# Performance work log

Hardware: AMD Instinct MI355X
Metric: run time of the kernel (lower is better)

## Reference

```python
import jax, jax.numpy as jnp
import numpy as np

B, LQ, LF, NW, NFR, E, D, V = 4, 128, 64, 2, 8, 128, 128, 64


def _project(x, W, b):
    # torch Emb_Projection('linear'): Linear then zero-row mask
    y = x @ W + b
    m = 1.0 - jnp.all(y == 0, axis=-1, keepdims=True).astype(y.dtype)
    return y * m


def setup_inputs() -> dict:
    key = jax.random.key(0)
    ks = jax.random.split(key, 12)
    s = lambda k, shape, fan: jax.random.normal(k, shape, jnp.float32) / np.sqrt(fan)
    return {
        "query": jax.random.normal(ks[0], (B, LQ, E), jnp.float32),
        "fragment": jax.random.normal(ks[1], (B, NW, NFR, LF, E), jnp.float32),
        "query_mask": jnp.ones((B, LQ), jnp.float32),
        "fragment_mask": jnp.ones((B, NW, NFR, LF), jnp.float32),
        # learned params (stored [in, out]; torch Linear is x @ W.T with W [out,in])
        "proj_W": s(ks[2], (E, D), E),
        "proj_b": jnp.zeros((D,), jnp.float32),
        "self_att_W": s(ks[3], (NW, D), D),   # n_way Linear(D,1,bias=False)
        "q_att_W": s(ks[4], (D, V), D),
        "f_att_W": s(ks[5], (D, V), D),
        "qf_att_W": s(ks[6], (D, V), D),
        "gate_w": s(ks[7], (V,), V),          # value_gate: Linear(V,1,bias=False)
        "val_w": s(ks[8], (V,), V),           # value_att:  Linear(V,1,bias=False)
    }


def reference(query, fragment, query_mask, fragment_mask, proj_W, proj_b,
              self_att_W, q_att_W, f_att_W, qf_att_W, gate_w, val_w):
    query = _project(query, proj_W, proj_b)          # [B,Lq,D]
    fragment = _project(fragment, proj_W, proj_b)    # [B,NW,NFR,Lf,D]

    # (1) fragment self-attention -> frag_code
    logits = jnp.einsum('bwfld,wd->bwfl', fragment, self_att_W)   # per-way Linear(D,1)
    e = jnp.exp(logits) * fragment_mask
    frag_self_att = e / (e.sum(-1, keepdims=True) + 1e-7)          # [B,NW,NFR,Lf]
    frag_code = (fragment * frag_self_att[..., None]).sum(-2)     # [B,NW,NFR,D]

    # (2) query-to-fragment attention
    frag_r = fragment.reshape(fragment.shape[0], -1, fragment.shape[-2], fragment.shape[-1])  # [B,NF,Lf,D]
    qr = query[:, None]                                            # [B,1,Lq,D]
    q_att = qr @ q_att_W                                           # [B,1,Lq,V]
    f_att = frag_r @ f_att_W                                       # [B,NF,Lf,V]
    # large broadcast product [B,NF,Lf,Lq,D] then project to V
    qf = (qr[:, :, None, :, :] * frag_r[:, :, :, None, :]) @ qf_att_W  # [B,NF,Lf,Lq,V]
    qf = q_att[:, :, None] + f_att[:, :, :, None] + qf
    qf = qf.max(axis=-3)                                           # max over Lf -> [B,NF,Lq,V]

    qf_gate = jax.nn.sigmoid(qf @ gate_w) * query_mask[:, None]    # [B,NF,Lq]
    e2 = jnp.exp(qf @ val_w) * query_mask[:, None]
    qf_norm = e2 / (e2.sum(-1, keepdims=True) + 1e-7)              # [B,NF,Lq]

    query_code = (qr * qf_norm[..., None]).sum(axis=2)             # [B,NF,D]
    query_code = query_code.reshape(frag_code.shape)               # [B,NW,NFR,D]
    return frag_code, query_code, frag_self_att, qf_gate, query
```

## Files before the change

kernel.cpp:

```cpp
#include <hip/hip_runtime.h>
#include <hip/hip_bf16.h>

#define B_   4
#define LQ_  128
#define LF_  64
#define NW_  2
#define NFR_ 8
#define E_   128
#define D_   128
#define V_   64
#define NWF_ (NW_*NFR_)
#define NROW_Q (B_*LQ_)
#define NROW_F (B_*NW_*NFR_*LF_)

using bf16 = __hip_bfloat16;
typedef unsigned short u16;
typedef unsigned int   u32;
typedef __attribute__((ext_vector_type(8))) short  bf16x8;
typedef __attribute__((ext_vector_type(4))) float  f32x4;
typedef __attribute__((ext_vector_type(4))) u32    u32x4;

#define WS_QP    0
#define WS_QATT  65536
#define WS_E2    98304
#define WS_FP16  106496
#define WS_W3T   368640
#define WS_WFT   372736
#define WS_PWT   376832
#define WS_QAT   385024

#define OUT_FRAGCODE  0
#define OUT_QUERYCODE 8192
#define OUT_SELFATT   16384
#define OUT_QFGATE    20480
#define OUT_QUERY     28672

__device__ __forceinline__ float us2f(u16 v) { return __uint_as_float((u32)v << 16); }
__device__ __forceinline__ float lo2f(u32 v) { return __uint_as_float(v << 16); }
__device__ __forceinline__ float hi2f(u32 v) { return __uint_as_float(v & 0xffff0000u); }
__device__ __forceinline__ u16 f2b_raw(float f) {
    u32 u = __float_as_uint(f);
    return (u16)((u + 0x7fffu + ((u >> 16) & 1u)) >> 16);
}
__device__ __forceinline__ u32 pk2(float hi, float lo) {
    return __builtin_amdgcn_perm(__float_as_uint(hi), __float_as_uint(lo), 0x07060302u);
}
template<bool BF> __device__ __forceinline__ float LD(const void* p, int i) {
    return BF ? us2f(((const u16*)p)[i]) : ((const float*)p)[i];
}
template<bool BF> __device__ __forceinline__ void ST(void* p, int i, float v) {
    if (BF) ((u16*)p)[i] = f2b_raw(v); else ((float*)p)[i] = v;
}
template<bool BF> __device__ __forceinline__ u16 LDB(const void* p, int i) {
    return BF ? ((const u16*)p)[i] : f2b_raw(((const float*)p)[i]);
}
__device__ __forceinline__ bool is_bf(const void* qmask) {
    return ((const u16*)qmask)[0] == 0x3F80u;
}

template<bool BF>
__device__ __forceinline__ void prep_body(const void* src, u16* dst, u16* stg, int N)
{
    int t = threadIdx.x;
    int st = N + 1, total = 128 * N;
    for (int i = t; i < total; i += 256)
        stg[(i / N) * st + (i % N)] = LDB<BF>(src, i);
    __syncthreads();
    for (int j = t; j < total; j += 256) {
        int n = j >> 7, k = j & 127;
        dst[n * 128 + k] = stg[k * st + n];
    }
}
__global__ __launch_bounds__(256) void k_prep(
    const void* projW, const void* qattW, const void* qfW, const void* fattW,
    const void* qmask, float* ws)
{
    __shared__ u16 stg[128 * 129];
    int bx = blockIdx.x;
    const void* src = (bx == 0) ? projW : (bx == 1) ? qattW : (bx == 2) ? qfW : fattW;
    u16* dst = (u16*)(ws + ((bx == 0) ? WS_PWT : (bx == 1) ? WS_QAT : (bx == 2) ? WS_W3T : WS_WFT));
    int N = (bx == 0) ? 128 : 64;
    if (is_bf(qmask)) prep_body<true >(src, dst, stg, N);
    else              prep_body<false>(src, dst, stg, N);
}

template<bool BF>
__device__ __forceinline__ void proj_body(
    const void* query, const void* fragment, const void* projB,
    float* ws, void* out, u16* s_y)
{
    int r = blockIdx.x, t = threadIdx.x;
    int lane = t & 63, wave = t >> 6, m = lane & 15, quad = lane >> 4;
    bool isq = (r >= 256);
    int base = isq ? (r - 256) * 16 : r * 16;
    const void* x = isq ? query : fragment;
    const u16* pwt = (const u16*)(ws + WS_PWT);

    bf16x8 af[4];
    #pragma unroll
    for (int kt = 0; kt < 4; ++kt) {
        int off = (base + m) * 128 + kt * 32 + quad * 8;
        if (BF) af[kt] = *(const bf16x8*)((const u16*)x + off);
        else {
            f32x4 a = *(const f32x4*)((const float*)x + off);
            f32x4 c = *(const f32x4*)((const float*)x + off + 4);
            u32x4 av;
            av.x = pk2(a.y, a.x); av.y = pk2(a.w, a.z);
            av.z = pk2(c.y, c.x); av.w = pk2(c.w, c.z);
            af[kt] = __builtin_bit_cast(bf16x8, av);
        }
    }
    int nt0 = wave * 2;
    f32x4 acc[2];
    #pragma unroll
    for (int i = 0; i < 2; ++i) {
        float bv = LD<BF>(projB, (nt0 + i) * 16 + m);
        acc[i] = (f32x4){bv, bv, bv, bv};
    }
    #pragma unroll
    for (int kt = 0; kt < 4; ++kt)
        #pragma unroll
        for (int i = 0; i < 2; ++i) {
            bf16x8 bfr = *(const bf16x8*)(pwt + ((nt0 + i) * 16 + m) * 128 + kt * 32 + quad * 8);
            acc[i] = __builtin_amdgcn_mfma_f32_16x16x32_bf16(af[kt], bfr, acc[i], 0, 0, 0);
        }
    if (!isq) {
        u16* fp16 = (u16*)(ws + WS_FP16);
        #pragma unroll
        for (int i = 0; i < 2; ++i)
            #pragma unroll
            for (int rr = 0; rr < 4; ++rr)
                fp16[(size_t)(base + quad * 4 + rr) * 128 + (nt0 + i) * 16 + m] = f2b_raw(acc[i][rr]);
    } else {
        #pragma unroll
        for (int i = 0; i < 2; ++i)
            #pragma unroll
            for (int rr = 0; rr < 4; ++rr) {
                int gr = base + quad * 4 + rr, col = (nt0 + i) * 16 + m;
                float v = acc[i][rr];
                ws[WS_QP + (size_t)gr * 128 + col] = v;
                ST<BF>(out, OUT_QUERY + gr * 128 + col, v);
                s_y[(quad * 4 + rr) * 132 + col] = f2b_raw(v);
            }
        __syncthreads();
        bf16x8 ay[4];
        #pragma unroll
        for (int kt = 0; kt < 4; ++kt)
            ay[kt] = *(const bf16x8*)&s_y[m * 132 + kt * 32 + quad * 8];
        const u16* qat = (const u16*)(ws + WS_QAT);
        f32x4 a2 = (f32x4){0.f, 0.f, 0.f, 0.f};
        #pragma unroll
        for (int kt = 0; kt < 4; ++kt) {
            bf16x8 b2 = *(const bf16x8*)(qat + (wave * 16 + m) * 128 + kt * 32 + quad * 8);
            a2 = __builtin_amdgcn_mfma_f32_16x16x32_bf16(ay[kt], b2, a2, 0, 0, 0);
        }
        #pragma unroll
        for (int rr = 0; rr < 4; ++rr)
            ws[WS_QATT + (size_t)(base + quad * 4 + rr) * 64 + wave * 16 + m] = a2[rr];
    }
}
__global__ __launch_bounds__(256) void k_proj(
    const void* query, const void* fragment, const void* projB, const void* qmask,
    float* ws, void* out)
{
    __shared__ u16 s_y[16 * 132];
    if (is_bf(qmask)) proj_body<true >(query, fragment, projB, ws, out, s_y);
    else              proj_body<false>(query, fragment, projB, ws, out, s_y);
}

template<bool BF>
__device__ __forceinline__ void qf_body(
    const void* saW, const void* fmask, const void* gatew, const void* valw,
    const void* qmask, float* ws, void* out, char* smem)
{
    u16*   s_fp  = (u16*)smem;
    u16*   s_fa  = (u16*)(smem + 16384);
    float* s_saw = (float*)(smem + 34816);
    float* s_att = (float*)(smem + 35328);
    float* s_tmp = (float*)(smem + 35584);

    int t = threadIdx.x, lane = t & 63, wave = t >> 6;
    int bwf = blockIdx.x >> 2, qt2 = blockIdx.x & 3;
    int b = bwf >> 4;
    int m = lane & 15, quad = lane >> 4;
    int lq = wave >> 1, qsub = wave & 1;
    int sk = (m & 7) << 3;

    {
        const u32* src = (const u32*)((const u16*)(ws + WS_FP16)) + (size_t)bwf * 4096;
        u32* d32 = (u32*)s_fp;
        #pragma unroll
        for (int k = 0; k < 16; ++k) {
            int i = t + 512 * k;
            int row = i >> 6, cp = i & 63;
            d32[row * 64 + (cp ^ ((row & 7) << 2))] = src[i];
        }
    }
    const u16* w3t = (const u16*)(ws + WS_W3T);
    bf16x8 w3f[4][4];
    #pragma unroll
    for (int vt = 0; vt < 4; ++vt)
        #pragma unroll
        for (int kt = 0; kt < 4; ++kt)
            w3f[vt][kt] = *(const bf16x8*)(w3t + (vt * 16 + m) * 128 + kt * 32 + quad * 8);
    __syncthreads();

    int lbase = lq * 16;
    if (qsub == 0) {
        const u16* wft = (const u16*)(ws + WS_WFT);
        bf16x8 afk[4];
        #pragma unroll
        for (int kt = 0; kt < 4; ++kt)
            afk[kt] = *(const bf16x8*)&s_fp[(lbase + m) * 128 + ((kt * 32 + quad * 8) ^ sk)];
        #pragma unroll
        for (int vt = 0; vt < 4; ++vt) {
            bf16x8 wf = *(const bf16x8*)(wft + (vt * 16 + m) * 128 + 0 * 32 + quad * 8);
            f32x4 a0 = (f32x4){0.f, 0.f, 0.f, 0.f};
            #pragma unroll
            for (int kt = 0; kt < 4; ++kt) {
                bf16x8 wk = *(const bf16x8*)(wft + (vt * 16 + m) * 128 + kt * 32 + quad * 8);
                a0 = __builtin_amdgcn_mfma_f32_16x16x32_bf16(afk[kt], wk, a0, 0, 0, 0);
                (void)wf;
            }
            #pragma unroll
            for (int r = 0; r < 4; ++r)
                s_fa[(lbase + quad * 4 + r) * 72 + vt * 16 + m] = f2b_raw(a0[r]);
        }
    }
    float qpreg[4][8];
    {
        const float* qprow = ws + WS_QP + (size_t)(b * LQ_ + qt2 * 32 + qsub * 16 + m) * 128;
        #pragma unroll
        for (int kt = 0; kt < 4; ++kt) {
            f32x4 x0 = *(const f32x4*)(qprow + kt * 32 + quad * 8);
            f32x4 x1 = *(const f32x4*)(qprow + kt * 32 + quad * 8 + 4);
            qpreg[kt][0] = x0.x; qpreg[kt][1] = x0.y; qpreg[kt][2] = x0.z; qpreg[kt][3] = x0.w;
            qpreg[kt][4] = x1.x; qpreg[kt][5] = x1.y; qpreg[kt][6] = x1.z; qpreg[kt][7] = x1.w;
        }
    }
    __syncthreads();

    float mx[4][4];
    #pragma unroll
    for (int vt = 0; vt < 4; ++vt)
        #pragma unroll
        for (int r = 0; r < 4; ++r) mx[vt][r] = -1e30f;

    u32x4 fvc[4], fvn[4];
    #pragma unroll
    for (int kt = 0; kt < 4; ++kt)
        fvc[kt] = *(const u32x4*)&s_fp[lbase * 128 + (kt * 32 + quad * 8)];
    #pragma unroll 2
    for (int li = 0; li < 16; ++li) {
        if (li < 15) {
            int l2 = lbase + li + 1;
            #pragma unroll
            for (int kt = 0; kt < 4; ++kt)
                fvn[kt] = *(const u32x4*)&s_fp[l2 * 128 + ((kt * 32 + quad * 8) ^ (((li + 1) & 7) << 3))];
        }
        int l = lbase + li;
        bf16x8 af[4];
        #pragma unroll
        for (int kt = 0; kt < 4; ++kt) {
            u32x4 fv = fvc[kt];
            u32x4 av;
            av.x = pk2(qpreg[kt][1] * hi2f(fv.x), qpreg[kt][0] * lo2f(fv.x));
            av.y = pk2(qpreg[kt][3] * hi2f(fv.y), qpreg[kt][2] * lo2f(fv.y));
            av.z = pk2(qpreg[kt][5] * hi2f(fv.z), qpreg[kt][4] * lo2f(fv.z));
            av.w = pk2(qpreg[kt][7] * hi2f(fv.w), qpreg[kt][6] * lo2f(fv.w));
            af[kt] = __builtin_bit_cast(bf16x8, av);
        }
        #pragma unroll
        for (int vt = 0; vt < 4; ++vt) {
            float fa = us2f(s_fa[l * 72 + vt * 16 + m]);
            f32x4 acc = (f32x4){fa, fa, fa, fa};
            #pragma unroll
            for (int kt = 0; kt < 4; ++kt)
                acc = __builtin_amdgcn_mfma_f32_16x16x32_bf16(af[kt], w3f[vt][kt], acc, 0, 0, 0);
            #pragma unroll
            for (int r = 0; r < 4; ++r) mx[vt][r] = fmaxf(mx[vt][r], acc[r]);
        }
        #pragma unroll
        for (int kt = 0; kt < 4; ++kt) fvc[kt] = fvn[kt];
    }
    __syncthreads();
    #pragma unroll
    for (int vt = 0; vt < 4; ++vt)
        #pragma unroll
        for (int r = 0; r < 4; ++r)
            s_fa[(lq * 32 + qsub * 16 + quad * 4 + r) * 72 + vt * 16 + m] = f2b_raw(mx[vt][r]);
    __syncthreads();

    {
        int q = t >> 4, vg = t & 15;
        int gq = qt2 * 32 + q;
        float gp = 0.f, ep = 0.f;
        #pragma unroll
        for (int jj = 0; jj < 4; ++jj) {
            int v = vg * 4 + jj;
            float mval = -1e30f;
            #pragma unroll
            for (int w = 0; w < 4; ++w)
                mval = fmaxf(mval, us2f(s_fa[(w * 32 + q) * 72 + v]));
            float qf = mval + ws[WS_QATT + (size_t)(b * LQ_ + gq) * 64 + v];
            gp += qf * LD<BF>(gatew, v);
            ep += qf * LD<BF>(valw, v);
        }
        #pragma unroll
        for (int off = 1; off <= 8; off <<= 1) {
            gp += __shfl_xor(gp, off, 64);
            ep += __shfl_xor(ep, off, 64);
        }
        if (vg == 0) {
            float qm = LD<BF>(qmask, b * LQ_ + gq);
            float g = (1.0f / (1.0f + expf(-gp))) * qm;
            ST<BF>(out, OUT_QFGATE + bwf * LQ_ + gq, g);
            ws[WS_E2 + bwf * LQ_ + gq] = expf(ep) * qm;
        }
    }

    if (qt2 == 0) {
        if (t < 128) s_saw[t] = LD<BF>(saW, ((bwf >> 3) & 1) * 128 + t);
        __syncthreads();
        int l = t >> 3, j8 = t & 7;
        int swz = (l & 7) << 3;
        float p = 0.f;
        #pragma unroll
        for (int seg = 0; seg < 2; ++seg) {
            int koff = j8 * 16 + seg * 8;
            u32x4 fv = *(const u32x4*)&s_fp[l * 128 + (koff ^ swz)];
            const float* swp = &s_saw[koff];
            p += lo2f(fv.x) * swp[0] + hi2f(fv.x) * swp[1]
               + lo2f(fv.y) * swp[2] + hi2f(fv.y) * swp[3]
               + lo2f(fv.z) * swp[4] + hi2f(fv.z) * swp[5]
               + lo2f(fv.w) * swp[6] + hi2f(fv.w) * swp[7];
        }
        p += __shfl_xor(p, 1, 64);
        p += __shfl_xor(p, 2, 64);
        p += __shfl_xor(p, 4, 64);
        if (j8 == 0) s_att[l] = expf(p) * LD<BF>(fmask, bwf * LF_ + l);
        __syncthreads();
        if (t < 64) {
            float e = s_att[t], s = e;
            #pragma unroll
            for (int off = 1; off <= 32; off <<= 1) s += __shfl_xor(s, off, 64);
            float nrm = e / (s + 1e-7f);
            s_att[t] = nrm;
            ST<BF>(out, OUT_SELFATT + bwf * LF_ + t, nrm);
        }
        __syncthreads();
        int d = t & 127, grp = t >> 7;
        float fc = 0.f;
        #pragma unroll
        for (int li2 = 0; li2 < 16; ++li2) {
            int l2 = grp * 16 + li2;
            fc += us2f(s_fp[l2 * 128 + (d ^ ((l2 & 7) << 3))]) * s_att[l2];
        }
        s_tmp[grp * 128 + d] = fc;
        __syncthreads();
        if (t < 128)
            ST<BF>(out, OUT_FRAGCODE + bwf * D_ + t,
                   s_tmp[t] + s_tmp[128 + t] + s_tmp[256 + t] + s_tmp[384 + t]);
    }
}
__global__ __launch_bounds__(512) void k_qf(
    const void* saW, const void* fmask, const void* gatew, const void* valw,
    const void* qmask, float* ws, void* out)
{
    __shared__ char smem[37632];
    if (is_bf(qmask)) qf_body<true >(saW, fmask, gatew, valw, qmask, ws, out, smem);
    else              qf_body<false>(saW, fmask, gatew, valw, qmask, ws, out, smem);
}

template<bool BF>
__device__ __forceinline__ void qcode_body(const float* ws, void* out,
                                           float* s_n, float* s_part)
{
    int bwf = blockIdx.x, b = bwf >> 4, t = threadIdx.x;
    float e = ws[WS_E2 + bwf * LQ_ + t];
    float s = e;
    #pragma unroll
    for (int off = 1; off <= 32; off <<= 1) s += __shfl_xor(s, off, 64);
    if ((t & 63) == 0) s_part[t >> 6] = s;
    __syncthreads();
    float tot = s_part[0] + s_part[1] + 1e-7f;
    s_n[t] = e / tot;
    __syncthreads();
    float qc = 0.f;
    #pragma unroll 8
    for (int q = 0; q < LQ_; ++q)
        qc += ws[WS_QP + (size_t)(b * LQ_ + q) * 128 + t] * s_n[q];
    ST<BF>(out, OUT_QUERYCODE + bwf * D_ + t, qc);
}
__global__ __launch_bounds__(128) void k_qcode(const void* qmask, const float* ws, void* out)
{
    __shared__ float s_n[LQ_];
    __shared__ float s_part[2];
    if (is_bf(qmask)) qcode_body<true >(ws, out, s_n, s_part);
    else              qcode_body<false>(ws, out, s_n, s_part);
}

extern "C" void kernel_launch(void* const* d_in, const int* in_sizes, int n_in,
                              void* d_out, int out_size, void* d_ws, size_t ws_size,
                              hipStream_t stream)
{
    const void* query    = d_in[0];
    const void* fragment = d_in[1];
    const void* qmask    = d_in[2];
    const void* fmask    = d_in[3];
    const void* projW    = d_in[4];
    const void* projB    = d_in[5];
    const void* saW      = d_in[6];
    const void* qattW    = d_in[7];
    const void* fattW    = d_in[8];
    const void* qfW      = d_in[9];
    const void* gatew    = d_in[10];
    const void* valw     = d_in[11];
    float* ws = (float*)d_ws;

    hipLaunchKernelGGL(k_prep, dim3(4), dim3(256), 0, stream,
                       projW, qattW, qfW, fattW, qmask, ws);
    hipLaunchKernelGGL(k_proj, dim3(288), dim3(256), 0, stream,
                       query, fragment, projB, qmask, ws, d_out);
    hipLaunchKernelGGL(k_qf, dim3(256), dim3(512), 0, stream,
                       saW, fmask, gatew, valw, qmask, ws, d_out);
    hipLaunchKernelGGL(k_qcode, dim3(B_ * NWF_), dim3(128), 0, stream,
                       qmask, ws, d_out);
}
```

Measured before the change: 114.2 us.

## Fuse all four kernels into one per-fragment block kernel

Replaces the prep, projection, qf and qcode kernels with a single kernel that launches one 512-thread block per (batch, fragment). Each block recomputes the query projection for its batch, projects its own fragment, and keeps everything in shared memory, so there are no workspace round trips and no extra launches. It also reads weights directly with strided gathers instead of using pre-transposed copies. The trade-offs are redundant query-projection work across the 16 blocks of each batch, a drop from 256 blocks to 64 (less parallelism), and each wave now looping over all 64 fragment rows rather than 16.

```diff
diff --git a/kernel.cpp b/kernel.cpp
--- a/kernel.cpp
+++ b/kernel.cpp
@@ -10,8 +10,6 @@
 #define D_   128
 #define V_   64
 #define NWF_ (NW_*NFR_)
-#define NROW_Q (B_*LQ_)
-#define NROW_F (B_*NW_*NFR_*LF_)
 
 using bf16 = __hip_bfloat16;
 typedef unsigned short u16;
@@ -20,20 +18,22 @@
 typedef __attribute__((ext_vector_type(4))) float  f32x4;
 typedef __attribute__((ext_vector_type(4))) u32    u32x4;
 
-#define WS_QP    0
-#define WS_QATT  65536
-#define WS_E2    98304
-#define WS_FP16  106496
-#define WS_W3T   368640
-#define WS_WFT   372736
-#define WS_PWT   376832
-#define WS_QAT   385024
-
 #define OUT_FRAGCODE  0
 #define OUT_QUERYCODE 8192
 #define OUT_SELFATT   16384
 #define OUT_QFGATE    20480
 #define OUT_QUERY     28672
+
+#define L_FP   0
+#define L_QP   16384
+#define L_FA   49152
+#define L_E2   58368
+#define L_N    58880
+#define L_SAW  59392
+#define L_ATT  59904
+#define L_RED  60160
+#define L_PART 62208
+#define L_TOT  62240
 
 __device__ __forceinline__ float us2f(u16 v) { return __uint_as_float((u32)v << 16); }
 __device__ __forceinline__ float lo2f(u32 v) { return __uint_as_float(v << 16); }
@@ -57,212 +57,152 @@
 __device__ __forceinline__ bool is_bf(const void* qmask) {
     return ((const u16*)qmask)[0] == 0x3F80u;
 }
-
 template<bool BF>
-__device__ __forceinline__ void prep_body(const void* src, u16* dst, u16* stg, int N)
+__device__ __forceinline__ bf16x8 loadA(const void* x, int row, int kt, int quad) {
+    int off = row * 128 + kt * 32 + quad * 8;
+    if (BF) return *(const bf16x8*)((const u16*)x + off);
+    f32x4 a = *(const f32x4*)((const float*)x + off);
+    f32x4 c = *(const f32x4*)((const float*)x + off + 4);
+    u32x4 av;
+    av.x = pk2(a.y, a.x); av.y = pk2(a.w, a.z);
+    av.z = pk2(c.y, c.x); av.w = pk2(c.w, c.z);
+    return __builtin_bit_cast(bf16x8, av);
+}
+template<bool BF>
+__device__ __forceinline__ bf16x8 ldBf(const void* W, int N, int n, int k0) {
+    short tmp[8];
+    #pragma unroll
+    for (int j = 0; j < 8; ++j) tmp[j] = (short)LDB<BF>(W, (k0 + j) * N + n);
+    bf16x8 f;
+    #pragma unroll
+    for (int j = 0; j < 8; ++j) f[j] = tmp[j];
+    return f;
+}
+
+template<bool BF>
+__device__ __forceinline__ void main_body(
+    const void* query, const void* fragment, const void* qmask, const void* fmask,
+    const void* projW, const void* projB, const void* saW, const void* qattW,
+    const void* fattW, const void* qfW, const void* gatew, const void* valw,
+    void* out, char* smem)
 {
-    int t = threadIdx.x;
-    int st = N + 1, total = 128 * N;
-    for (int i = t; i < total; i += 256)
-        stg[(i / N) * st + (i % N)] = LDB<BF>(src, i);
-    __syncthreads();
-    for (int j = t; j < total; j += 256) {
-        int n = j >> 7, k = j & 127;
-        dst[n * 128 + k] = stg[k * st + n];
-    }
-}
-__global__ __launch_bounds__(256) void k_prep(
-    const void* projW, const void* qattW, const void* qfW, const void* fattW,
-    const void* qmask, float* ws)
-{
-    __shared__ u16 stg[128 * 129];
-    int bx = blockIdx.x;
-    const void* src = (bx == 0) ? projW : (bx == 1) ? qattW : (bx == 2) ? qfW : fattW;
-    u16* dst = (u16*)(ws + ((bx == 0) ? WS_PWT : (bx == 1) ? WS_QAT : (bx == 2) ? WS_W3T : WS_WFT));
-    int N = (bx == 0) ? 128 : 64;
-    if (is_bf(qmask)) prep_body<true >(src, dst, stg, N);
-    else              prep_body<false>(src, dst, stg, N);
-}
-
-template<bool BF>
-__device__ __forceinline__ void proj_body(
-    const void* query, const void* fragment, const void* projB,
-    float* ws, void* out, u16* s_y)
-{
-    int r = blockIdx.x, t = threadIdx.x;
-    int lane = t & 63, wave = t >> 6, m = lane & 15, quad = lane >> 4;
-    bool isq = (r >= 256);
-    int base = isq ? (r - 256) * 16 : r * 16;
-    const void* x = isq ? query : fragment;
-    const u16* pwt = (const u16*)(ws + WS_PWT);
-
-    bf16x8 af[4];
+    u16*   s_fp   = (u16*)(smem + L_FP);
+    u16*   s_qp   = (u16*)(smem + L_QP);
+    u16*   s_fa   = (u16*)(smem + L_FA);
+    float* s_e2   = (float*)(smem + L_E2);
+    float* s_n    = (float*)(smem + L_N);
+    float* s_saw  = (float*)(smem + L_SAW);
+    float* s_att  = (float*)(smem + L_ATT);
+    float* s_red  = (float*)(smem + L_RED);
+    float* s_part = (float*)(smem + L_PART);
+
+    int bwf = blockIdx.x, b = bwf >> 4;
+    int t = threadIdx.x, lane = t & 63, w = t >> 6;
+    int m = lane & 15, quad = lane >> 4;
+    int sk = (m & 7) << 3;
+
+    {
+        bool dofp = (w < 4);
+        bf16x8 af_q[4], af_f[4];
+        #pragma unroll
+        for (int kt = 0; kt < 4; ++kt)
+            af_q[kt] = loadA<BF>(query, b * 128 + w * 16 + m, kt, quad);
+        if (dofp)
+            #pragma unroll
+            for (int kt = 0; kt < 4; ++kt)
+                af_f[kt] = loadA<BF>(fragment, bwf * 64 + w * 16 + m, kt, quad);
+        #pragma unroll
+        for (int nt = 0; nt < 8; ++nt) {
+            int n = nt * 16 + m;
+            bf16x8 bw[4];
+            #pragma unroll
+            for (int kt = 0; kt < 4; ++kt) bw[kt] = ldBf<BF>(projW, 128, n, kt * 32 + quad * 8);
+            float bv = LD<BF>(projB, n);
+            f32x4 aq = (f32x4){bv, bv, bv, bv};
+            #pragma unroll
+            for (int kt = 0; kt < 4; ++kt)
+                aq = __builtin_amdgcn_mfma_f32_16x16x32_bf16(af_q[kt], bw[kt], aq, 0, 0, 0);
+            #pragma unroll
+            for (int rr = 0; rr < 4; ++rr) {
+                int row = w * 16 + quad * 4 + rr;
+                s_qp[row * 128 + (n ^ ((row & 7) << 3))] = f2b_raw(aq[rr]);
+            }
+            if (dofp) {
+                f32x4 afc = (f32x4){bv, bv, bv, bv};
+                #pragma unroll
+                for (int kt = 0; kt < 4; ++kt)
+                    afc = __builtin_amdgcn_mfma_f32_16x16x32_bf16(af_f[kt], bw[kt], afc, 0, 0, 0);
+                #pragma unroll
+                for (int rr = 0; rr < 4; ++rr) {
+                    int row = w * 16 + quad * 4 + rr;
+                    s_fp[row * 128 + (n ^ ((row & 7) << 3))] = f2b_raw(afc[rr]);
+                }
+            }
+        }
+    }
+    __syncthreads();
+
+    bf16x8 aq2[4];
+    #pragma unroll
+    for (int kt = 0; kt < 4; ++kt)
+        aq2[kt] = *(const bf16x8*)&s_qp[(w * 16 + m) * 128 + ((kt * 32 + quad * 8) ^ sk)];
+    f32x4 qat[4];
+    #pragma unroll
+    for (int vt = 0; vt < 4; ++vt) {
+        qat[vt] = (f32x4){0.f, 0.f, 0.f, 0.f};
+        #pragma unroll
+        for (int kt = 0; kt < 4; ++kt) {
+            bf16x8 bb = ldBf<BF>(qattW, 64, vt * 16 + m, kt * 32 + quad * 8);
+            qat[vt] = __builtin_amdgcn_mfma_f32_16x16x32_bf16(aq2[kt], bb, qat[vt], 0, 0, 0);
+        }
+    }
+    float qpreg[4][8];
     #pragma unroll
     for (int kt = 0; kt < 4; ++kt) {
-        int off = (base + m) * 128 + kt * 32 + quad * 8;
-        if (BF) af[kt] = *(const bf16x8*)((const u16*)x + off);
-        else {
-            f32x4 a = *(const f32x4*)((const float*)x + off);
-            f32x4 c = *(const f32x4*)((const float*)x + off + 4);
-            u32x4 av;
-            av.x = pk2(a.y, a.x); av.y = pk2(a.w, a.z);
-            av.z = pk2(c.y, c.x); av.w = pk2(c.w, c.z);
-            af[kt] = __builtin_bit_cast(bf16x8, av);
-        }
-    }
-    int nt0 = wave * 2;
-    f32x4 acc[2];
-    #pragma unroll
-    for (int i = 0; i < 2; ++i) {
-        float bv = LD<BF>(projB, (nt0 + i) * 16 + m);
-        acc[i] = (f32x4){bv, bv, bv, bv};
-    }
-    #pragma unroll
-    for (int kt = 0; kt < 4; ++kt)
-        #pragma unroll
-        for (int i = 0; i < 2; ++i) {
-            bf16x8 bfr = *(const bf16x8*)(pwt + ((nt0 + i) * 16 + m) * 128 + kt * 32 + quad * 8);
-            acc[i] = __builtin_amdgcn_mfma_f32_16x16x32_bf16(af[kt], bfr, acc[i], 0, 0, 0);
-        }
-    if (!isq) {
-        u16* fp16 = (u16*)(ws + WS_FP16);
-        #pragma unroll
-        for (int i = 0; i < 2; ++i)
-            #pragma unroll
-            for (int rr = 0; rr < 4; ++rr)
-                fp16[(size_t)(base + quad * 4 + rr) * 128 + (nt0 + i) * 16 + m] = f2b_raw(acc[i][rr]);
-    } else {
-        #pragma unroll
-        for (int i = 0; i < 2; ++i)
-            #pragma unroll
-            for (int rr = 0; rr < 4; ++rr) {
-                int gr = base + quad * 4 + rr, col = (nt0 + i) * 16 + m;
-                float v = acc[i][rr];
-                ws[WS_QP + (size_t)gr * 128 + col] = v;
-                ST<BF>(out, OUT_QUERY + gr * 128 + col, v);
-                s_y[(quad * 4 + rr) * 132 + col] = f2b_raw(v);
-            }
-        __syncthreads();
-        bf16x8 ay[4];
+        u32x4 uv = __builtin_bit_cast(u32x4, aq2[kt]);
+        qpreg[kt][0] = lo2f(uv.x); qpreg[kt][1] = hi2f(uv.x);
+        qpreg[kt][2] = lo2f(uv.y); qpreg[kt][3] = hi2f(uv.y);
+        qpreg[kt][4] = lo2f(uv.z); qpreg[kt][5] = hi2f(uv.z);
+        qpreg[kt][6] = lo2f(uv.w); qpreg[kt][7] = hi2f(uv.w);
+    }
+    if (w < 4) {
+        bf16x8 afa[4];
         #pragma unroll
         for (int kt = 0; kt < 4; ++kt)
-            ay[kt] = *(const bf16x8*)&s_y[m * 132 + kt * 32 + quad * 8];
-        const u16* qat = (const u16*)(ws + WS_QAT);
-        f32x4 a2 = (f32x4){0.f, 0.f, 0.f, 0.f};
+            afa[kt] = *(const bf16x8*)&s_fp[(w * 16 + m) * 128 + ((kt * 32 + quad * 8) ^ sk)];
+        #pragma unroll
+        for (int vt = 0; vt < 4; ++vt) {
+            f32x4 a0 = (f32x4){0.f, 0.f, 0.f, 0.f};
+            #pragma unroll
+            for (int kt = 0; kt < 4; ++kt) {
+                bf16x8 wk = ldBf<BF>(fattW, 64, vt * 16 + m, kt * 32 + quad * 8);
+                a0 = __builtin_amdgcn_mfma_f32_16x16x32_bf16(afa[kt], wk, a0, 0, 0, 0);
+            }
+            #pragma unroll
+            for (int r = 0; r < 4; ++r)
+                s_fa[(w * 16 + quad * 4 + r) * 72 + vt * 16 + m] = f2b_raw(a0[r]);
+        }
+    }
+    bf16x8 w3f[4][4];
+    #pragma unroll
+    for (int vt = 0; vt < 4; ++vt)
+        #pragma unroll
+        for (int kt = 0; kt < 4; ++kt)
+            w3f[vt][kt] = ldBf<BF>(qfW, 64, vt * 16 + m, kt * 32 + quad * 8);
+    __syncthreads();
+
+    float mx[4][4];
+    #pragma unroll
+    for (int vt = 0; vt < 4; ++vt)
+        #pragma unroll
+        for (int r = 0; r < 4; ++r) mx[vt][r] = -1e30f;
+    #pragma unroll 2
+    for (int li = 0; li < 64; ++li) {
+        int sw2 = (li & 7) << 3;
+        bf16x8 af[4];
         #pragma unroll
         for (int kt = 0; kt < 4; ++kt) {
-            bf16x8 b2 = *(const bf16x8*)(qat + (wave * 16 + m) * 128 + kt * 32 + quad * 8);
-            a2 = __builtin_amdgcn_mfma_f32_16x16x32_bf16(ay[kt], b2, a2, 0, 0, 0);
-        }
-        #pragma unroll
-        for (int rr = 0; rr < 4; ++rr)
-            ws[WS_QATT + (size_t)(base + quad * 4 + rr) * 64 + wave * 16 + m] = a2[rr];
-    }
-}
-__global__ __launch_bounds__(256) void k_proj(
-    const void* query, const void* fragment, const void* projB, const void* qmask,
-    float* ws, void* out)
-{
-    __shared__ u16 s_y[16 * 132];
-    if (is_bf(qmask)) proj_body<true >(query, fragment, projB, ws, out, s_y);
-    else              proj_body<false>(query, fragment, projB, ws, out, s_y);
-}
-
-template<bool BF>
-__device__ __forceinline__ void qf_body(
-    const void* saW, const void* fmask, const void* gatew, const void* valw,
-    const void* qmask, float* ws, void* out, char* smem)
-{
-    u16*   s_fp  = (u16*)smem;
-    u16*   s_fa  = (u16*)(smem + 16384);
-    float* s_saw = (float*)(smem + 34816);
-    float* s_att = (float*)(smem + 35328);
-    float* s_tmp = (float*)(smem + 35584);
-
-    int t = threadIdx.x, lane = t & 63, wave = t >> 6;
-    int bwf = blockIdx.x >> 2, qt2 = blockIdx.x & 3;
-    int b = bwf >> 4;
-    int m = lane & 15, quad = lane >> 4;
-    int lq = wave >> 1, qsub = wave & 1;
-    int sk = (m & 7) << 3;
-
-    {
-        const u32* src = (const u32*)((const u16*)(ws + WS_FP16)) + (size_t)bwf * 4096;
-        u32* d32 = (u32*)s_fp;
-        #pragma unroll
-        for (int k = 0; k < 16; ++k) {
-            int i = t + 512 * k;
-            int row = i >> 6, cp = i & 63;
-            d32[row * 64 + (cp ^ ((row & 7) << 2))] = src[i];
-        }
-    }
-    const u16* w3t = (const u16*)(ws + WS_W3T);
-    bf16x8 w3f[4][4];
-    #pragma unroll
-    for (int vt = 0; vt < 4; ++vt)
-        #pragma unroll
-        for (int kt = 0; kt < 4; ++kt)
-            w3f[vt][kt] = *(const bf16x8*)(w3t + (vt * 16 + m) * 128 + kt * 32 + quad * 8);
-    __syncthreads();
-
-    int lbase = lq * 16;
-    if (qsub == 0) {
-        const u16* wft = (const u16*)(ws + WS_WFT);
-        bf16x8 afk[4];
-        #pragma unroll
-        for (int kt = 0; kt < 4; ++kt)
-            afk[kt] = *(const bf16x8*)&s_fp[(lbase + m) * 128 + ((kt * 32 + quad * 8) ^ sk)];
-        #pragma unroll
-        for (int vt = 0; vt < 4; ++vt) {
-            bf16x8 wf = *(const bf16x8*)(wft + (vt * 16 + m) * 128 + 0 * 32 + quad * 8);
-            f32x4 a0 = (f32x4){0.f, 0.f, 0.f, 0.f};
-            #pragma unroll
-            for (int kt = 0; kt < 4; ++kt) {
-                bf16x8 wk = *(const bf16x8*)(wft + (vt * 16 + m) * 128 + kt * 32 + quad * 8);
-                a0 = __builtin_amdgcn_mfma_f32_16x16x32_bf16(afk[kt], wk, a0, 0, 0, 0);
-                (void)wf;
-            }
-            #pragma unroll
-            for (int r = 0; r < 4; ++r)
-                s_fa[(lbase + quad * 4 + r) * 72 + vt * 16 + m] = f2b_raw(a0[r]);
-        }
-    }
-    float qpreg[4][8];
-    {
-        const float* qprow = ws + WS_QP + (size_t)(b * LQ_ + qt2 * 32 + qsub * 16 + m) * 128;
-        #pragma unroll
-        for (int kt = 0; kt < 4; ++kt) {
-            f32x4 x0 = *(const f32x4*)(qprow + kt * 32 + quad * 8);
-            f32x4 x1 = *(const f32x4*)(qprow + kt * 32 + quad * 8 + 4);
-            qpreg[kt][0] = x0.x; qpreg[kt][1] = x0.y; qpreg[kt][2] = x0.z; qpreg[kt][3] = x0.w;
-            qpreg[kt][4] = x1.x; qpreg[kt][5] = x1.y; qpreg[kt][6] = x1.z; qpreg[kt][7] = x1.w;
-        }
-    }
-    __syncthreads();
-
-    float mx[4][4];
-    #pragma unroll
-    for (int vt = 0; vt < 4; ++vt)
-        #pragma unroll
-        for (int r = 0; r < 4; ++r) mx[vt][r] = -1e30f;
-
-    u32x4 fvc[4], fvn[4];
-    #pragma unroll
-    for (int kt = 0; kt < 4; ++kt)
-        fvc[kt] = *(const u32x4*)&s_fp[lbase * 128 + (kt * 32 + quad * 8)];
-    #pragma unroll 2
-    for (int li = 0; li < 16; ++li) {
-        if (li < 15) {
-            int l2 = lbase + li + 1;
-            #pragma unroll
-            for (int kt = 0; kt < 4; ++kt)
-                fvn[kt] = *(const u32x4*)&s_fp[l2 * 128 + ((kt * 32 + quad * 8) ^ (((li + 1) & 7) << 3))];
-        }
-        int l = lbase + li;
-        bf16x8 af[4];
-        #pragma unroll
-        for (int kt = 0; kt < 4; ++kt) {
-            u32x4 fv = fvc[kt];
+            u32x4 fv = *(const u32x4*)&s_fp[li * 128 + ((kt * 32 + quad * 8) ^ sw2)];
             u32x4 av;
             av.x = pk2(qpreg[kt][1] * hi2f(fv.x), qpreg[kt][0] * lo2f(fv.x));
             av.y = pk2(qpreg[kt][3] * hi2f(fv.y), qpreg[kt][2] * lo2f(fv.y));
@@ -272,7 +212,7 @@
         }
         #pragma unroll
         for (int vt = 0; vt < 4; ++vt) {
-            float fa = us2f(s_fa[l * 72 + vt * 16 + m]);
+            float fa = us2f(s_fa[li * 72 + vt * 16 + m]);
             f32x4 acc = (f32x4){fa, fa, fa, fa};
             #pragma unroll
             for (int kt = 0; kt < 4; ++kt)
@@ -280,48 +220,52 @@
             #pragma unroll
             for (int r = 0; r < 4; ++r) mx[vt][r] = fmaxf(mx[vt][r], acc[r]);
         }
-        #pragma unroll
-        for (int kt = 0; kt < 4; ++kt) fvc[kt] = fvn[kt];
-    }
-    __syncthreads();
-    #pragma unroll
-    for (int vt = 0; vt < 4; ++vt)
-        #pragma unroll
-        for (int r = 0; r < 4; ++r)
-            s_fa[(lq * 32 + qsub * 16 + quad * 4 + r) * 72 + vt * 16 + m] = f2b_raw(mx[vt][r]);
-    __syncthreads();
-
-    {
-        int q = t >> 4, vg = t & 15;
-        int gq = qt2 * 32 + q;
-        float gp = 0.f, ep = 0.f;
-        #pragma unroll
-        for (int jj = 0; jj < 4; ++jj) {
-            int v = vg * 4 + jj;
-            float mval = -1e30f;
-            #pragma unroll
-            for (int w = 0; w < 4; ++w)
-                mval = fmaxf(mval, us2f(s_fa[(w * 32 + q) * 72 + v]));
-            float qf = mval + ws[WS_QATT + (size_t)(b * LQ_ + gq) * 64 + v];
-            gp += qf * LD<BF>(gatew, v);
-            ep += qf * LD<BF>(valw, v);
-        }
-        #pragma unroll
-        for (int off = 1; off <= 8; off <<= 1) {
-            gp += __shfl_xor(gp, off, 64);
-            ep += __shfl_xor(ep, off, 64);
-        }
-        if (vg == 0) {
-            float qm = LD<BF>(qmask, b * LQ_ + gq);
-            float g = (1.0f / (1.0f + expf(-gp))) * qm;
-            ST<BF>(out, OUT_QFGATE + bwf * LQ_ + gq, g);
-            ws[WS_E2 + bwf * LQ_ + gq] = expf(ep) * qm;
-        }
-    }
-
-    if (qt2 == 0) {
-        if (t < 128) s_saw[t] = LD<BF>(saW, ((bwf >> 3) & 1) * 128 + t);
-        __syncthreads();
+    }
+
+    {
+        float gwv[4], vwv[4];
+        #pragma unroll
+        for (int vt = 0; vt < 4; ++vt) {
+            gwv[vt] = LD<BF>(gatew, vt * 16 + m);
+            vwv[vt] = LD<BF>(valw, vt * 16 + m);
+        }
+        #pragma unroll
+        for (int r = 0; r < 4; ++r) {
+            float gp = 0.f, ep = 0.f;
+            #pragma unroll
+            for (int vt = 0; vt < 4; ++vt) {
+                float qf = mx[vt][r] + qat[vt][r];
+                gp += qf * gwv[vt];
+                ep += qf * vwv[vt];
+            }
+            #pragma unroll
+            for (int off = 1; off <= 8; off <<= 1) {
+                gp += __shfl_xor(gp, off, 64);
+                ep += __shfl_xor(ep, off, 64);
+            }
+            if (m == 0) {
+                int gq = w * 16 + quad * 4 + r;
+                float qm = LD<BF>(qmask, b * 128 + gq);
+                float g = (1.0f / (1.0f + expf(-gp))) * qm;
+                ST<BF>(out, OUT_QFGATE + bwf * LQ_ + gq, g);
+                s_e2[gq] = expf(ep) * qm;
+            }
+        }
+    }
+
+    if ((bwf & 15) == 0) {
+        #pragma unroll
+        for (int it = 0; it < 32; ++it) {
+            int i = t + 512 * it;
+            int row = i >> 7, col = i & 127;
+            float v = us2f(s_qp[row * 128 + (col ^ ((row & 7) << 3))]);
+            ST<BF>(out, OUT_QUERY + (b * 128 + row) * 128 + col, v);
+        }
+    }
+
+    if (t < 128) s_saw[t] = LD<BF>(saW, ((bwf >> 3) & 1) * 128 + t);
+    __syncthreads();
+    {
         int l = t >> 3, j8 = t & 7;
         int swz = (l & 7) << 3;
         float p = 0.f;
@@ -339,16 +283,18 @@
         p += __shfl_xor(p, 2, 64);
         p += __shfl_xor(p, 4, 64);
         if (j8 == 0) s_att[l] = expf(p) * LD<BF>(fmask, bwf * LF_ + l);
-        __syncthreads();
-        if (t < 64) {
-            float e = s_att[t], s = e;
-            #pragma unroll
-            for (int off = 1; off <= 32; off <<= 1) s += __shfl_xor(s, off, 64);
-            float nrm = e / (s + 1e-7f);
-            s_att[t] = nrm;
-            ST<BF>(out, OUT_SELFATT + bwf * LF_ + t, nrm);
-        }
-        __syncthreads();
+    }
+    __syncthreads();
+    if (t < 64) {
+        float e = s_att[t], s = e;
+        #pragma unroll
+        for (int off = 1; off <= 32; off <<= 1) s += __shfl_xor(s, off, 64);
+        float nrm = e / (s + 1e-7f);
+        s_att[t] = nrm;
+        ST<BF>(out, OUT_SELFATT + bwf * LF_ + t, nrm);
+    }
+    __syncthreads();
+    {
         int d = t & 127, grp = t >> 7;
         float fc = 0.f;
         #pragma unroll
@@ -356,74 +302,65 @@
             int l2 = grp * 16 + li2;
             fc += us2f(s_fp[l2 * 128 + (d ^ ((l2 & 7) << 3))]) * s_att[l2];
         }
-        s_tmp[grp * 128 + d] = fc;
-        __syncthreads();
-        if (t < 128)
-            ST<BF>(out, OUT_FRAGCODE + bwf * D_ + t,
-                   s_tmp[t] + s_tmp[128 + t] + s_tmp[256 + t] + s_tmp[384 + t]);
-    }
-}
-__global__ __launch_bounds__(512) void k_qf(
-    const void* saW, const void* fmask, const void* gatew, const void* valw,
-    const void* qmask, float* ws, void* out)
+        s_red[grp * 128 + d] = fc;
+    }
+    __syncthreads();
+    if (t < 128)
+        ST<BF>(out, OUT_FRAGCODE + bwf * D_ + t,
+               s_red[t] + s_red[128 + t] + s_red[256 + t] + s_red[384 + t]);
+
+    float e2v = 0.f;
+    if (t < 128) {
+        e2v = s_e2[t];
+        float s = e2v;
+        #pragma unroll
+        for (int off = 1; off <= 32; off <<= 1) s += __shfl_xor(s, off, 64);
+        if (lane == 0) s_part[w] = s;
+    }
+    __syncthreads();
+    if (t < 128) {
+        float tot = s_part[0] + s_part[1] + 1e-7f;
+        s_n[t] = e2v / tot;
+    }
+    __syncthreads();
+
+    {
+        int d = t & 127, qg = t >> 7;
+        float qc = 0.f;
+        #pragma unroll
+        for (int qi = 0; qi < 32; ++qi) {
+            int q = qg * 32 + qi;
+            qc += us2f(s_qp[q * 128 + (d ^ ((q & 7) << 3))]) * s_n[q];
+        }
+        s_red[qg * 128 + d] = qc;
+    }
+    __syncthreads();
+    if (t < 128)
+        ST<BF>(out, OUT_QUERYCODE + bwf * D_ + t,
+               s_red[t] + s_red[128 + t] + s_red[256 + t] + s_red[384 + t]);
+}
+
+__global__ __launch_bounds__(512, 2) void k_main(
+    const void* query, const void* fragment, const void* qmask, const void* fmask,
+    const void* projW, const void* projB, const void* saW, const void* qattW,
+    const void* fattW, const void* qfW, const void* gatew, const void* valw,
+    void* out)
 {
-    __shared__ char smem[37632];
-    if (is_bf(qmask)) qf_body<true >(saW, fmask, gatew, valw, qmask, ws, out, smem);
-    else              qf_body<false>(saW, fmask, gatew, valw, qmask, ws, out, smem);
-}
-
-template<bool BF>
-__device__ __forceinline__ void qcode_body(const float* ws, void* out,
-                                           float* s_n, float* s_part)
-{
-    int bwf = blockIdx.x, b = bwf >> 4, t = threadIdx.x;
-    float e = ws[WS_E2 + bwf * LQ_ + t];
-    float s = e;
-    #pragma unroll
-    for (int off = 1; off <= 32; off <<= 1) s += __shfl_xor(s, off, 64);
-    if ((t & 63) == 0) s_part[t >> 6] = s;
-    __syncthreads();
-    float tot = s_part[0] + s_part[1] + 1e-7f;
-    s_n[t] = e / tot;
-    __syncthreads();
-    float qc = 0.f;
-    #pragma unroll 8
-    for (int q = 0; q < LQ_; ++q)
-        qc += ws[WS_QP + (size_t)(b * LQ_ + q) * 128 + t] * s_n[q];
-    ST<BF>(out, OUT_QUERYCODE + bwf * D_ + t, qc);
-}
-__global__ __launch_bounds__(128) void k_qcode(const void* qmask, const float* ws, void* out)
-{
-    __shared__ float s_n[LQ_];
-    __shared__ float s_part[2];
-    if (is_bf(qmask)) qcode_body<true >(ws, out, s_n, s_part);
-    else              qcode_body<false>(ws, out, s_n, s_part);
+    __shared__ char smem[L_TOT];
+    if (is_bf(qmask))
+        main_body<true >(query, fragment, qmask, fmask, projW, projB, saW, qattW,
+                         fattW, qfW, gatew, valw, out, smem);
+    else
+        main_body<false>(query, fragment, qmask, fmask, projW, projB, saW, qattW,
+                         fattW, qfW, gatew, valw, out, smem);
 }
 
 extern "C" void kernel_launch(void* const* d_in, const int* in_sizes, int n_in,
                               void* d_out, int out_size, void* d_ws, size_t ws_size,
                               hipStream_t stream)
 {
-    const void* query    = d_in[0];
-    const void* fragment = d_in[1];
-    const void* qmask    = d_in[2];
-    const void* fmask    = d_in[3];
-    const void* projW    = d_in[4];
-    const void* projB    = d_in[5];
-    const void* saW      = d_in[6];
-    const void* qattW    = d_in[7];
-    const void* fattW    = d_in[8];
-    const void* qfW      = d_in[9];
-    const void* gatew    = d_in[10];
-    const void* valw     = d_in[11];
-    float* ws = (float*)d_ws;
-
-    hipLaunchKernelGGL(k_prep, dim3(4), dim3(256), 0, stream,
-                       projW, qattW, qfW, fattW, qmask, ws);
-    hipLaunchKernelGGL(k_proj, dim3(288), dim3(256), 0, stream,
-                       query, fragment, projB, qmask, ws, d_out);
-    hipLaunchKernelGGL(k_qf, dim3(256), dim3(512), 0, stream,
-                       saW, fmask, gatew, valw, qmask, ws, d_out);
-    hipLaunchKernelGGL(k_qcode, dim3(B_ * NWF_), dim3(128), 0, stream,
-                       qmask, ws, d_out);
-}
+    hipLaunchKernelGGL(k_main, dim3(B_ * NWF_), dim3(512), 0, stream,
+                       d_in[0], d_in[1], d_in[2], d_in[3], d_in[4], d_in[5],
+                       d_in[6], d_in[7], d_in[8], d_in[9], d_in[10], d_in[11],
+                       d_out);
+}
```

After: 125.0 us. 1.09x slower.
